# Kernel optimization log

Hardware: AMD Instinct MI355X
Metric: run time of the kernel (lower is better)

The kernel has to match this reference:

```python
import jax, jax.numpy as jnp
import numpy as np

T, H, I, E, K = 2048, 1024, 1024, 16, 4
ALPHA, LIMIT, EPS = 1.702, 7.0, 1e-5


def setup_inputs() -> dict:
    key = jax.random.key(0)
    ks = jax.random.split(key, 8)
    s = 0.02  # init scale for weights
    return {
        "x": jax.random.normal(ks[0], (T, H), jnp.float32),
        "norm_scale": jnp.ones((H,), jnp.float32),
        "gate_w": jax.random.normal(ks[1], (E, H), jnp.float32) * s,
        "gate_b": jax.random.normal(ks[2], (E,), jnp.float32) * s,
        "mlp1_w": jax.random.normal(ks[3], (E, 2 * I, H), jnp.float32) * s,
        "mlp1_b": jax.random.normal(ks[4], (E, 2 * I), jnp.float32) * s,
        "mlp2_w": jax.random.normal(ks[5], (E, H, I), jnp.float32) * s,
        "mlp2_b": jax.random.normal(ks[6], (E, H), jnp.float32) * s,
    }


def rmsnorm(x, scale):
    t = x * jax.lax.rsqrt(jnp.mean(x * x, axis=-1, keepdims=True) + EPS)
    return t * scale


def swiglu(h):
    # interleaved gating: even channels -> glu, odd channels -> linear
    glu = jnp.minimum(h[..., ::2], LIMIT)
    lin = jnp.clip(h[..., 1::2], -LIMIT, LIMIT)
    return glu * jax.nn.sigmoid(ALPHA * glu) * (lin + 1.0)


def reference(x, norm_scale, gate_w, gate_b, mlp1_w, mlp1_b, mlp2_w, mlp2_b):
    t = rmsnorm(x, norm_scale)                                   # [T,H]
    g = t @ gate_w.T + gate_b                                    # [T,E]
    vals, idx = jax.lax.top_k(g, K)                              # [T,K]
    w = jax.nn.softmax(vals, axis=-1)                            # [T,K]
    # Dense per-expert FFN (same math as per-token weight gather, computed
    # once per expert then selected -- avoids materializing [T,K,2I,H]).
    h = jnp.einsum('th,ech->tec', t, mlp1_w) + mlp1_b            # [T,E,2I]
    act = swiglu(h)                                              # [T,E,I]
    y = jnp.einsum('tei,ehi->teh', act, mlp2_w) + mlp2_b         # [T,E,H]
    y_sel = jnp.take_along_axis(y, idx[:, :, None], axis=1)      # [T,K,H]
    return x + jnp.einsum('tkh,tk->th', y_sel, w)
```

## Files before the change

### kernel.cpp

```cpp
#include <hip/hip_runtime.h>
#include <hip/hip_bf16.h>
#include <stdint.h>

typedef unsigned short u16;
typedef __attribute__((ext_vector_type(8))) short short8;
typedef __attribute__((ext_vector_type(4))) float f32x4;

#define T_TOK 2048
#define H_DIM 1024
#define E_NUM 16
#define TWO_I 2048
#define I_DIM 1024
#define ALPHA 1.702f
#define LIMIT 7.0f
#define CNT_STRIDE 64

__device__ __forceinline__ u16 f2b(float f) {
    uint32_t x = __builtin_bit_cast(uint32_t, f);
    uint32_t r = x + 0x7fffu + ((x >> 16) & 1u);
    return (u16)(r >> 16);
}
__device__ __forceinline__ short8 pack8(float4 a, float4 b) {
    short8 r;
    r[0] = (short)f2b(a.x); r[1] = (short)f2b(a.y);
    r[2] = (short)f2b(a.z); r[3] = (short)f2b(a.w);
    r[4] = (short)f2b(b.x); r[5] = (short)f2b(b.y);
    r[6] = (short)f2b(b.z); r[7] = (short)f2b(b.w);
    return r;
}

typedef __attribute__((address_space(1))) void gas_void;
typedef __attribute__((address_space(3))) void las_void;
__device__ __forceinline__ void gl_lds16(const void* g, void* l) {
    __builtin_amdgcn_global_load_lds((gas_void*)g, (las_void*)l, 16, 0, 0);
}

template<typename BT> struct BFrag;
template<> struct BFrag<u16> {
    short8 v;
    __device__ __forceinline__ void load(const u16* p) { v = *(const short8*)p; }
    __device__ __forceinline__ short8 get() const { return v; }
};
template<> struct BFrag<float> {
    float4 a, b;
    __device__ __forceinline__ void load(const float* p) {
        const float4* q = (const float4*)p; a = q[0]; b = q[1];
    }
    __device__ __forceinline__ short8 get() const { return pack8(a, b); }
};

__global__ __launch_bounds__(256) void cvt_kernel(
    const float* __restrict__ in1, u16* __restrict__ out1, int n1,
    const float* __restrict__ in2, u16* __restrict__ out2, int n2)
{
    int i = blockIdx.x * 256 + threadIdx.x;
    int stride = gridDim.x * 256;
    int ntot = n1 + n2;
    for (; i < ntot; i += stride) {
        const float* in; u16* out; int j;
        if (i < n1) { in = in1; out = out1; j = i; }
        else        { in = in2; out = out2; j = i - n1; }
        float4 v = ((const float4*)in)[j];
        uint32_t lo = (uint32_t)f2b(v.x) | ((uint32_t)f2b(v.y) << 16);
        uint32_t hi = (uint32_t)f2b(v.z) | ((uint32_t)f2b(v.w) << 16);
        uint2 p; p.x = lo; p.y = hi;
        ((uint2*)out)[j] = p;
    }
}

__global__ __launch_bounds__(256) void prep_kernel(
    const float* __restrict__ x, const float* __restrict__ scale,
    const float* __restrict__ gw, const float* __restrict__ gb,
    u16* __restrict__ t_out, int* __restrict__ cnt,
    int* __restrict__ pairs, float* __restrict__ pweight,
    float* __restrict__ out)
{
    const int t = blockIdx.x, tid = threadIdx.x;
    const int lane = tid & 63, wid = tid >> 6;
    __shared__ float red[4];
    __shared__ float g4[4][16];
    __shared__ float gsh[16];
    __shared__ float rstd_sh;

    const float4 xv = ((const float4*)(x + (size_t)t * H_DIM))[tid];
    ((float4*)(out + (size_t)t * H_DIM))[tid] = xv;
    float ss = xv.x*xv.x + xv.y*xv.y + xv.z*xv.z + xv.w*xv.w;
#pragma unroll
    for (int off = 32; off > 0; off >>= 1) ss += __shfl_down(ss, off);
    if (lane == 0) red[wid] = ss;
    __syncthreads();
    if (tid == 0) rstd_sh = rsqrtf((red[0]+red[1]+red[2]+red[3]) * (1.f/1024.f) + 1e-5f);
    __syncthreads();
    const float rstd = rstd_sh;
    const float4 sc = ((const float4*)scale)[tid];
    float4 tv;
    tv.x = xv.x * rstd * sc.x; tv.y = xv.y * rstd * sc.y;
    tv.z = xv.z * rstd * sc.z; tv.w = xv.w * rstd * sc.w;
    {
        uint32_t lo = (uint32_t)f2b(tv.x) | ((uint32_t)f2b(tv.y) << 16);
        uint32_t hi = (uint32_t)f2b(tv.z) | ((uint32_t)f2b(tv.w) << 16);
        uint2 p; p.x = lo; p.y = hi;
        *(uint2*)(t_out + (size_t)t * H_DIM + tid * 4) = p;
    }
    float part[16];
#pragma unroll
    for (int e = 0; e < 16; e++) {
        const float4 w4 = ((const float4*)(gw + (size_t)e * H_DIM))[tid];
        part[e] = tv.x*w4.x + tv.y*w4.y + tv.z*w4.z + tv.w*w4.w;
    }
#pragma unroll
    for (int e = 0; e < 16; e++) {
        float v = part[e];
#pragma unroll
        for (int off = 32; off > 0; off >>= 1) v += __shfl_down(v, off);
        if (lane == 0) g4[wid][e] = v;
    }
    __syncthreads();
    if (tid < 16) gsh[tid] = g4[0][tid] + g4[1][tid] + g4[2][tid] + g4[3][tid] + gb[tid];
    __syncthreads();
    if (tid == 0) {
        unsigned mask = 0;
        float vals[4]; int idxs[4];
#pragma unroll
        for (int k = 0; k < 4; k++) {
            float best = -1e30f; int bi = 0;
            for (int e = 0; e < 16; e++)
                if (!((mask >> e) & 1u) && gsh[e] > best) { best = gsh[e]; bi = e; }
            mask |= 1u << bi; vals[k] = best; idxs[k] = bi;
        }
        float m = vals[0], s = 0.f, w[4];
#pragma unroll
        for (int k = 0; k < 4; k++) { w[k] = __expf(vals[k] - m); s += w[k]; }
        float inv = 1.f / s;
#pragma unroll
        for (int k = 0; k < 4; k++) {
            int slot = atomicAdd(&cnt[idxs[k] * CNT_STRIDE], 1);
            pairs[idxs[k] * 2048 + slot] = t * 4 + k;
            pweight[t * 4 + k] = w[k] * inv;
        }
    }
}

template<typename BT>
__global__ __launch_bounds__(256, 1) void ffn1_kernel(
    const u16* __restrict__ t_ws, const BT* __restrict__ w1,
    const float* __restrict__ b1, const int* __restrict__ cnt,
    const int* __restrict__ pairs, u16* __restrict__ act)
{
    const int e = blockIdx.z, nt = blockIdx.x, mt = blockIdx.y;
    const int cnt_e = cnt[e * CNT_STRIDE];
    if (mt * 128 >= cnt_e) return;
    const int tid = threadIdx.x;

    __shared__ u16 As[128 * 64];
    __shared__ u16 Bs[128 * 64];

    const BT* w1e = w1 + (size_t)e * TWO_I * H_DIM;
    const int* plist = pairs + e * 2048;

    const u16* aptr[4]; const BT* bptr[4]; int ldsoff[4];
#pragma unroll
    for (int i = 0; i < 4; i++) {
        int c = tid + i * 256;
        int r = c >> 3, kc = c & 7;
        int kcs = kc ^ (r & 7);
        int gr = mt * 128 + r;
        int info = (gr < cnt_e) ? plist[gr] : plist[0];
        aptr[i] = t_ws + (size_t)(info >> 2) * H_DIM + kcs * 8;
        ldsoff[i] = c * 8;
        int t16 = r >> 4, l16 = r & 15;
        int hcol = nt * 128 + (t16 >> 1) * 32 + l16 * 2 + (t16 & 1);
        bptr[i] = w1e + (size_t)hcol * H_DIM + kcs * 8;
    }

    const int lane = tid & 63, wid = tid >> 6;
    const int wm = wid >> 1, wn = wid & 1;
    const int l15 = lane & 15, quad = lane >> 4;
    const int swz = l15 & 7;

    f32x4 acc[4][4];
#pragma unroll
    for (int mi = 0; mi < 4; mi++)
#pragma unroll
        for (int ni = 0; ni < 4; ni++) acc[mi][ni] = (f32x4){0.f, 0.f, 0.f, 0.f};

    for (int ki = 0; ki < 16; ki++) {
        __syncthreads();
        if constexpr (sizeof(BT) == 2) {
#pragma unroll
            for (int i = 0; i < 4; i++) gl_lds16(aptr[i] + ki * 64, &As[ldsoff[i]]);
#pragma unroll
            for (int i = 0; i < 4; i++) gl_lds16((const BT*)bptr[i] + ki * 64, &Bs[ldsoff[i]]);
        } else {
            short8 ta[4]; BFrag<BT> fb[4];
#pragma unroll
            for (int i = 0; i < 4; i++) ta[i] = *(const short8*)(aptr[i] + ki * 64);
#pragma unroll
            for (int i = 0; i < 4; i++) fb[i].load(bptr[i] + ki * 64);
#pragma unroll
            for (int i = 0; i < 4; i++) *(short8*)(&As[ldsoff[i]]) = ta[i];
#pragma unroll
            for (int i = 0; i < 4; i++) *(short8*)(&Bs[ldsoff[i]]) = fb[i].get();
        }
        __syncthreads();
#pragma unroll
        for (int ks = 0; ks < 2; ks++) {
            short8 af[4], bfr[4];
#pragma unroll
            for (int mi = 0; mi < 4; mi++)
                af[mi] = *(const short8*)(&As[(wm * 64 + mi * 16 + l15) * 64 + (((ks << 2) + quad) ^ swz) * 8]);
#pragma unroll
            for (int ni = 0; ni < 4; ni++)
                bfr[ni] = *(const short8*)(&Bs[(wn * 64 + ni * 16 + l15) * 64 + (((ks << 2) + quad) ^ swz) * 8]);
#pragma unroll
            for (int mi = 0; mi < 4; mi++)
#pragma unroll
                for (int ni = 0; ni < 4; ni++)
                    acc[mi][ni] = __builtin_amdgcn_mfma_f32_16x16x32_bf16(af[mi], bfr[ni], acc[mi][ni], 0, 0, 0);
        }
    }

#pragma unroll
    for (int mi = 0; mi < 4; mi++) {
        int rloc = wm * 64 + mi * 16 + quad * 4;
        int rinfo[4]; bool rval[4];
#pragma unroll
        for (int rg = 0; rg < 4; rg++) {
            int gr = mt * 128 + rloc + rg;
            rval[rg] = gr < cnt_e;
            rinfo[rg] = rval[rg] ? plist[gr] : 0;
        }
#pragma unroll
        for (int qi = 0; qi < 2; qi++) {
            int actcol = nt * 64 + (wn * 2 + qi) * 16 + l15;
            float be = b1[e * TWO_I + 2 * actcol];
            float bo = b1[e * TWO_I + 2 * actcol + 1];
            f32x4 De = acc[mi][qi * 2], Do = acc[mi][qi * 2 + 1];
#pragma unroll
            for (int rg = 0; rg < 4; rg++) {
                if (!rval[rg]) continue;
                float he = De[rg] + be, ho = Do[rg] + bo;
                float glu = fminf(he, LIMIT);
                float lin = fminf(fmaxf(ho, -LIMIT), LIMIT);
                float a = glu * (1.f / (1.f + __expf(-ALPHA * glu))) * (lin + 1.f);
                act[(size_t)rinfo[rg] * I_DIM + actcol] = f2b(a);
            }
        }
    }
}

template<typename BT>
__global__ __launch_bounds__(256, 1) void ffn2_kernel(
    const u16* __restrict__ act, const BT* __restrict__ w2,
    const float* __restrict__ b2, const int* __restrict__ cnt,
    const int* __restrict__ pairs, const float* __restrict__ pweight,
    float* __restrict__ out)
{
    const int e = blockIdx.z, nt = blockIdx.x, mt = blockIdx.y;
    const int cnt_e = cnt[e * CNT_STRIDE];
    if (mt * 128 >= cnt_e) return;
    const int tid = threadIdx.x;

    __shared__ u16 As[128 * 64];
    __shared__ u16 Bs[128 * 64];

    const BT* w2e = w2 + (size_t)e * H_DIM * I_DIM;
    const int* plist = pairs + e * 2048;

    const u16* aptr[4]; const BT* bptr[4]; int ldsoff[4];
#pragma unroll
    for (int i = 0; i < 4; i++) {
        int c = tid + i * 256;
        int r = c >> 3, kc = c & 7;
        int kcs = kc ^ (r & 7);
        int gr = mt * 128 + r;
        int info = (gr < cnt_e) ? plist[gr] : plist[0];
        aptr[i] = act + (size_t)info * I_DIM + kcs * 8;
        ldsoff[i] = c * 8;
        bptr[i] = w2e + (size_t)(nt * 128 + r) * I_DIM + kcs * 8;
    }

    const int lane = tid & 63, wid = tid >> 6;
    const int wm = wid >> 1, wn = wid & 1;
    const int l15 = lane & 15, quad = lane >> 4;
    const int swz = l15 & 7;

    f32x4 acc[4][4];
#pragma unroll
    for (int mi = 0; mi < 4; mi++)
#pragma unroll
        for (int ni = 0; ni < 4; ni++) acc[mi][ni] = (f32x4){0.f, 0.f, 0.f, 0.f};

    for (int ki = 0; ki < 16; ki++) {
        __syncthreads();
        if constexpr (sizeof(BT) == 2) {
#pragma unroll
            for (int i = 0; i < 4; i++) gl_lds16(aptr[i] + ki * 64, &As[ldsoff[i]]);
#pragma unroll
            for (int i = 0; i < 4; i++) gl_lds16((const BT*)bptr[i] + ki * 64, &Bs[ldsoff[i]]);
        } else {
            short8 ta[4]; BFrag<BT> fb[4];
#pragma unroll
            for (int i = 0; i < 4; i++) ta[i] = *(const short8*)(aptr[i] + ki * 64);
#pragma unroll
            for (int i = 0; i < 4; i++) fb[i].load(bptr[i] + ki * 64);
#pragma unroll
            for (int i = 0; i < 4; i++) *(short8*)(&As[ldsoff[i]]) = ta[i];
#pragma unroll
            for (int i = 0; i < 4; i++) *(short8*)(&Bs[ldsoff[i]]) = fb[i].get();
        }
        __syncthreads();
#pragma unroll
        for (int ks = 0; ks < 2; ks++) {
            short8 af[4], bfr[4];
#pragma unroll
            for (int mi = 0; mi < 4; mi++)
                af[mi] = *(const short8*)(&As[(wm * 64 + mi * 16 + l15) * 64 + (((ks << 2) + quad) ^ swz) * 8]);
#pragma unroll
            for (int ni = 0; ni < 4; ni++)
                bfr[ni] = *(const short8*)(&Bs[(wn * 64 + ni * 16 + l15) * 64 + (((ks << 2) + quad) ^ swz) * 8]);
#pragma unroll
            for (int mi = 0; mi < 4; mi++)
#pragma unroll
                for (int ni = 0; ni < 4; ni++)
                    acc[mi][ni] = __builtin_amdgcn_mfma_f32_16x16x32_bf16(af[mi], bfr[ni], acc[mi][ni], 0, 0, 0);
        }
    }

#pragma unroll
    for (int mi = 0; mi < 4; mi++) {
        int rloc = wm * 64 + mi * 16 + quad * 4;
        int rinfo[4]; bool rval[4]; float wp[4];
#pragma unroll
        for (int rg = 0; rg < 4; rg++) {
            int gr = mt * 128 + rloc + rg;
            rval[rg] = gr < cnt_e;
            rinfo[rg] = rval[rg] ? plist[gr] : 0;
            wp[rg] = rval[rg] ? pweight[rinfo[rg]] : 0.f;
        }
#pragma unroll
        for (int ni = 0; ni < 4; ni++) {
            int hc = nt * 128 + wn * 64 + ni * 16 + l15;
            float bv = b2[e * H_DIM + hc];
#pragma unroll
            for (int rg = 0; rg < 4; rg++) {
                if (!rval[rg]) continue;
                float val = (acc[mi][ni][rg] + bv) * wp[rg];
                atomicAdd(&out[(size_t)(rinfo[rg] >> 2) * H_DIM + hc], val);
            }
        }
    }
}

extern "C" void kernel_launch(void* const* d_in, const int* in_sizes, int n_in,
                              void* d_out, int out_size, void* d_ws, size_t ws_size,
                              hipStream_t stream)
{
    const float* x      = (const float*)d_in[0];
    const float* nscale = (const float*)d_in[1];
    const float* gate_w = (const float*)d_in[2];
    const float* gate_b = (const float*)d_in[3];
    const float* mlp1_w = (const float*)d_in[4];
    const float* mlp1_b = (const float*)d_in[5];
    const float* mlp2_w = (const float*)d_in[6];
    const float* mlp2_b = (const float*)d_in[7];
    float* out = (float*)d_out;

    char* ws = (char*)d_ws;
    u16*   t_ws  = (u16*)(ws);
    u16*   act   = (u16*)(ws + (4ull << 20));
    int*   cnt   = (int*)(ws + (28ull << 20));
    int*   pairs = (int*)(ws + (28ull << 20) + 4096);
    float* pw    = (float*)(ws + (28ull << 20) + 4096 + E_NUM * 2048 * 4);
    u16*   w1b   = (u16*)(ws + (32ull << 20));
    u16*   w2b   = (u16*)(ws + (96ull << 20));

    const bool big = ws_size >= (128ull << 20);

    hipMemsetAsync(cnt, 0, E_NUM * CNT_STRIDE * sizeof(int), stream);

    if (big) {
        cvt_kernel<<<2048, 256, 0, stream>>>(mlp1_w, w1b, E_NUM * TWO_I * H_DIM / 4,
                                             mlp2_w, w2b, E_NUM * H_DIM * I_DIM / 4);
    }
    prep_kernel<<<T_TOK, 256, 0, stream>>>(x, nscale, gate_w, gate_b, t_ws, cnt, pairs, pw, out);
    if (big) {
        ffn1_kernel<u16><<<dim3(16, 16, E_NUM), 256, 0, stream>>>(t_ws, w1b, mlp1_b, cnt, pairs, act);
        ffn2_kernel<u16><<<dim3(8, 16, E_NUM), 256, 0, stream>>>(act, w2b, mlp2_b, cnt, pairs, pw, out);
    } else {
        ffn1_kernel<float><<<dim3(16, 16, E_NUM), 256, 0, stream>>>(t_ws, mlp1_w, mlp1_b, cnt, pairs, act);
        ffn2_kernel<float><<<dim3(8, 16, E_NUM), 256, 0, stream>>>(act, mlp2_w, mlp2_b, cnt, pairs, pw, out);
    }
}
```

Baseline: 437.3 us.

## Enlarge FFN GEMM tiles to 256x256 with 512 threads and double-buffered LDS

Both expert GEMM kernels move from 128x128 tiles with 256 threads to 256x256 tiles with 8 waves, each wave holding an 8x4 grid of MFMA accumulators. The global-to-LDS loads are now double-buffered, so the next K slice is prefetched while the current one is computed, and one barrier per iteration is removed. The weight conversion kernel also processes 8 floats per thread with 16-byte stores. The larger tiles improve operand reuse but sharply cut the block count (fewer M tiles per expert, more wasted rows on partial tiles), raise register pressure from 128 accumulator floats, and use 128 KB of LDS.

```diff
diff --git a/kernel.cpp b/kernel.cpp
--- a/kernel.cpp
+++ b/kernel.cpp
@@ -55,16 +55,19 @@
 {
     int i = blockIdx.x * 256 + threadIdx.x;
     int stride = gridDim.x * 256;
-    int ntot = n1 + n2;
-    for (; i < ntot; i += stride) {
+    int p1 = n1 >> 1, ptot = (n1 + n2) >> 1;
+    for (; i < ptot; i += stride) {
         const float* in; u16* out; int j;
-        if (i < n1) { in = in1; out = out1; j = i; }
-        else        { in = in2; out = out2; j = i - n1; }
-        float4 v = ((const float4*)in)[j];
-        uint32_t lo = (uint32_t)f2b(v.x) | ((uint32_t)f2b(v.y) << 16);
-        uint32_t hi = (uint32_t)f2b(v.z) | ((uint32_t)f2b(v.w) << 16);
-        uint2 p; p.x = lo; p.y = hi;
-        ((uint2*)out)[j] = p;
+        if (i < p1) { in = in1; out = out1; j = i; }
+        else        { in = in2; out = out2; j = i - p1; }
+        float4 a = ((const float4*)in)[2 * j];
+        float4 b = ((const float4*)in)[2 * j + 1];
+        uint4 p;
+        p.x = (uint32_t)f2b(a.x) | ((uint32_t)f2b(a.y) << 16);
+        p.y = (uint32_t)f2b(a.z) | ((uint32_t)f2b(a.w) << 16);
+        p.z = (uint32_t)f2b(b.x) | ((uint32_t)f2b(b.y) << 16);
+        p.w = (uint32_t)f2b(b.z) | ((uint32_t)f2b(b.w) << 16);
+        ((uint4*)out)[j] = p;
     }
 }
 
@@ -142,18 +145,18 @@
 }
 
 template<typename BT>
-__global__ __launch_bounds__(256, 1) void ffn1_kernel(
+__global__ __launch_bounds__(512, 1) void ffn1_kernel(
     const u16* __restrict__ t_ws, const BT* __restrict__ w1,
     const float* __restrict__ b1, const int* __restrict__ cnt,
     const int* __restrict__ pairs, u16* __restrict__ act)
 {
     const int e = blockIdx.z, nt = blockIdx.x, mt = blockIdx.y;
     const int cnt_e = cnt[e * CNT_STRIDE];
-    if (mt * 128 >= cnt_e) return;
+    if (mt * 256 >= cnt_e) return;
     const int tid = threadIdx.x;
 
-    __shared__ u16 As[128 * 64];
-    __shared__ u16 Bs[128 * 64];
+    __shared__ u16 As[2][256 * 64];
+    __shared__ u16 Bs[2][256 * 64];
 
     const BT* w1e = w1 + (size_t)e * TWO_I * H_DIM;
     const int* plist = pairs + e * 2048;
@@ -161,78 +164,79 @@
     const u16* aptr[4]; const BT* bptr[4]; int ldsoff[4];
 #pragma unroll
     for (int i = 0; i < 4; i++) {
-        int c = tid + i * 256;
+        int c = tid + i * 512;
         int r = c >> 3, kc = c & 7;
         int kcs = kc ^ (r & 7);
-        int gr = mt * 128 + r;
+        int gr = mt * 256 + r;
         int info = (gr < cnt_e) ? plist[gr] : plist[0];
         aptr[i] = t_ws + (size_t)(info >> 2) * H_DIM + kcs * 8;
         ldsoff[i] = c * 8;
         int t16 = r >> 4, l16 = r & 15;
-        int hcol = nt * 128 + (t16 >> 1) * 32 + l16 * 2 + (t16 & 1);
+        int hcol = nt * 256 + (t16 >> 1) * 32 + l16 * 2 + (t16 & 1);
         bptr[i] = w1e + (size_t)hcol * H_DIM + kcs * 8;
     }
 
     const int lane = tid & 63, wid = tid >> 6;
-    const int wm = wid >> 1, wn = wid & 1;
+    const int wm = wid >> 2, wn = wid & 3;
     const int l15 = lane & 15, quad = lane >> 4;
     const int swz = l15 & 7;
 
-    f32x4 acc[4][4];
-#pragma unroll
-    for (int mi = 0; mi < 4; mi++)
+    f32x4 acc[8][4];
+#pragma unroll
+    for (int mi = 0; mi < 8; mi++)
 #pragma unroll
         for (int ni = 0; ni < 4; ni++) acc[mi][ni] = (f32x4){0.f, 0.f, 0.f, 0.f};
 
+    auto stage = [&](int ki, int buf) {
+#pragma unroll
+        for (int i = 0; i < 4; i++) gl_lds16(aptr[i] + ki * 64, &As[buf][ldsoff[i]]);
+        if constexpr (sizeof(BT) == 2) {
+#pragma unroll
+            for (int i = 0; i < 4; i++) gl_lds16((const u16*)bptr[i] + ki * 64, &Bs[buf][ldsoff[i]]);
+        } else {
+            BFrag<BT> fb[4];
+#pragma unroll
+            for (int i = 0; i < 4; i++) fb[i].load(bptr[i] + ki * 64);
+#pragma unroll
+            for (int i = 0; i < 4; i++) *(short8*)(&Bs[buf][ldsoff[i]]) = fb[i].get();
+        }
+    };
+
+    stage(0, 0);
+    __syncthreads();
     for (int ki = 0; ki < 16; ki++) {
+        const int cur = ki & 1;
+        if (ki < 15) stage(ki + 1, cur ^ 1);
+#pragma unroll
+        for (int ks = 0; ks < 2; ks++) {
+            short8 bfr[4];
+#pragma unroll
+            for (int ni = 0; ni < 4; ni++)
+                bfr[ni] = *(const short8*)(&Bs[cur][(wn * 64 + ni * 16 + l15) * 64 + (((ks << 2) + quad) ^ swz) * 8]);
+#pragma unroll
+            for (int mi = 0; mi < 8; mi++) {
+                short8 af = *(const short8*)(&As[cur][(wm * 128 + mi * 16 + l15) * 64 + (((ks << 2) + quad) ^ swz) * 8]);
+#pragma unroll
+                for (int ni = 0; ni < 4; ni++)
+                    acc[mi][ni] = __builtin_amdgcn_mfma_f32_16x16x32_bf16(af, bfr[ni], acc[mi][ni], 0, 0, 0);
+            }
+        }
         __syncthreads();
-        if constexpr (sizeof(BT) == 2) {
-#pragma unroll
-            for (int i = 0; i < 4; i++) gl_lds16(aptr[i] + ki * 64, &As[ldsoff[i]]);
-#pragma unroll
-            for (int i = 0; i < 4; i++) gl_lds16((const BT*)bptr[i] + ki * 64, &Bs[ldsoff[i]]);
-        } else {
-            short8 ta[4]; BFrag<BT> fb[4];
-#pragma unroll
-            for (int i = 0; i < 4; i++) ta[i] = *(const short8*)(aptr[i] + ki * 64);
-#pragma unroll
-            for (int i = 0; i < 4; i++) fb[i].load(bptr[i] + ki * 64);
-#pragma unroll
-            for (int i = 0; i < 4; i++) *(short8*)(&As[ldsoff[i]]) = ta[i];
-#pragma unroll
-            for (int i = 0; i < 4; i++) *(short8*)(&Bs[ldsoff[i]]) = fb[i].get();
-        }
-        __syncthreads();
-#pragma unroll
-        for (int ks = 0; ks < 2; ks++) {
-            short8 af[4], bfr[4];
-#pragma unroll
-            for (int mi = 0; mi < 4; mi++)
-                af[mi] = *(const short8*)(&As[(wm * 64 + mi * 16 + l15) * 64 + (((ks << 2) + quad) ^ swz) * 8]);
-#pragma unroll
-            for (int ni = 0; ni < 4; ni++)
-                bfr[ni] = *(const short8*)(&Bs[(wn * 64 + ni * 16 + l15) * 64 + (((ks << 2) + quad) ^ swz) * 8]);
-#pragma unroll
-            for (int mi = 0; mi < 4; mi++)
-#pragma unroll
-                for (int ni = 0; ni < 4; ni++)
-                    acc[mi][ni] = __builtin_amdgcn_mfma_f32_16x16x32_bf16(af[mi], bfr[ni], acc[mi][ni], 0, 0, 0);
-        }
-    }
-
-#pragma unroll
-    for (int mi = 0; mi < 4; mi++) {
-        int rloc = wm * 64 + mi * 16 + quad * 4;
+    }
+
+#pragma unroll
+    for (int mi = 0; mi < 8; mi++) {
+        int rloc = wm * 128 + mi * 16 + quad * 4;
         int rinfo[4]; bool rval[4];
 #pragma unroll
         for (int rg = 0; rg < 4; rg++) {
-            int gr = mt * 128 + rloc + rg;
+            int gr = mt * 256 + rloc + rg;
             rval[rg] = gr < cnt_e;
             rinfo[rg] = rval[rg] ? plist[gr] : 0;
         }
 #pragma unroll
         for (int qi = 0; qi < 2; qi++) {
-            int actcol = nt * 64 + (wn * 2 + qi) * 16 + l15;
+            int actcol = nt * 128 + (wn * 2 + qi) * 16 + l15;
             float be = b1[e * TWO_I + 2 * actcol];
             float bo = b1[e * TWO_I + 2 * actcol + 1];
             f32x4 De = acc[mi][qi * 2], Do = acc[mi][qi * 2 + 1];
@@ -250,7 +254,7 @@
 }
 
 template<typename BT>
-__global__ __launch_bounds__(256, 1) void ffn2_kernel(
+__global__ __launch_bounds__(512, 1) void ffn2_kernel(
     const u16* __restrict__ act, const BT* __restrict__ w2,
     const float* __restrict__ b2, const int* __restrict__ cnt,
     const int* __restrict__ pairs, const float* __restrict__ pweight,
@@ -258,11 +262,11 @@
 {
     const int e = blockIdx.z, nt = blockIdx.x, mt = blockIdx.y;
     const int cnt_e = cnt[e * CNT_STRIDE];
-    if (mt * 128 >= cnt_e) return;
+    if (mt * 256 >= cnt_e) return;
     const int tid = threadIdx.x;
 
-    __shared__ u16 As[128 * 64];
-    __shared__ u16 Bs[128 * 64];
+    __shared__ u16 As[2][256 * 64];
+    __shared__ u16 Bs[2][256 * 64];
 
     const BT* w2e = w2 + (size_t)e * H_DIM * I_DIM;
     const int* plist = pairs + e * 2048;
@@ -270,77 +274,78 @@
     const u16* aptr[4]; const BT* bptr[4]; int ldsoff[4];
 #pragma unroll
     for (int i = 0; i < 4; i++) {
-        int c = tid + i * 256;
+        int c = tid + i * 512;
         int r = c >> 3, kc = c & 7;
         int kcs = kc ^ (r & 7);
-        int gr = mt * 128 + r;
+        int gr = mt * 256 + r;
         int info = (gr < cnt_e) ? plist[gr] : plist[0];
         aptr[i] = act + (size_t)info * I_DIM + kcs * 8;
         ldsoff[i] = c * 8;
-        bptr[i] = w2e + (size_t)(nt * 128 + r) * I_DIM + kcs * 8;
+        bptr[i] = w2e + (size_t)(nt * 256 + r) * I_DIM + kcs * 8;
     }
 
     const int lane = tid & 63, wid = tid >> 6;
-    const int wm = wid >> 1, wn = wid & 1;
+    const int wm = wid >> 2, wn = wid & 3;
     const int l15 = lane & 15, quad = lane >> 4;
     const int swz = l15 & 7;
 
-    f32x4 acc[4][4];
-#pragma unroll
-    for (int mi = 0; mi < 4; mi++)
+    f32x4 acc[8][4];
+#pragma unroll
+    for (int mi = 0; mi < 8; mi++)
 #pragma unroll
         for (int ni = 0; ni < 4; ni++) acc[mi][ni] = (f32x4){0.f, 0.f, 0.f, 0.f};
 
+    auto stage = [&](int ki, int buf) {
+#pragma unroll
+        for (int i = 0; i < 4; i++) gl_lds16(aptr[i] + ki * 64, &As[buf][ldsoff[i]]);
+        if constexpr (sizeof(BT) == 2) {
+#pragma unroll
+            for (int i = 0; i < 4; i++) gl_lds16((const u16*)bptr[i] + ki * 64, &Bs[buf][ldsoff[i]]);
+        } else {
+            BFrag<BT> fb[4];
+#pragma unroll
+            for (int i = 0; i < 4; i++) fb[i].load(bptr[i] + ki * 64);
+#pragma unroll
+            for (int i = 0; i < 4; i++) *(short8*)(&Bs[buf][ldsoff[i]]) = fb[i].get();
+        }
+    };
+
+    stage(0, 0);
+    __syncthreads();
     for (int ki = 0; ki < 16; ki++) {
+        const int cur = ki & 1;
+        if (ki < 15) stage(ki + 1, cur ^ 1);
+#pragma unroll
+        for (int ks = 0; ks < 2; ks++) {
+            short8 bfr[4];
+#pragma unroll
+            for (int ni = 0; ni < 4; ni++)
+                bfr[ni] = *(const short8*)(&Bs[cur][(wn * 64 + ni * 16 + l15) * 64 + (((ks << 2) + quad) ^ swz) * 8]);
+#pragma unroll
+            for (int mi = 0; mi < 8; mi++) {
+                short8 af = *(const short8*)(&As[cur][(wm * 128 + mi * 16 + l15) * 64 + (((ks << 2) + quad) ^ swz) * 8]);
+#pragma unroll
+                for (int ni = 0; ni < 4; ni++)
+                    acc[mi][ni] = __builtin_amdgcn_mfma_f32_16x16x32_bf16(af, bfr[ni], acc[mi][ni], 0, 0, 0);
+            }
+        }
         __syncthreads();
-        if constexpr (sizeof(BT) == 2) {
-#pragma unroll
-            for (int i = 0; i < 4; i++) gl_lds16(aptr[i] + ki * 64, &As[ldsoff[i]]);
-#pragma unroll
-            for (int i = 0; i < 4; i++) gl_lds16((const BT*)bptr[i] + ki * 64, &Bs[ldsoff[i]]);
-        } else {
-            short8 ta[4]; BFrag<BT> fb[4];
-#pragma unroll
-            for (int i = 0; i < 4; i++) ta[i] = *(const short8*)(aptr[i] + ki * 64);
-#pragma unroll
-            for (int i = 0; i < 4; i++) fb[i].load(bptr[i] + ki * 64);
-#pragma unroll
-            for (int i = 0; i < 4; i++) *(short8*)(&As[ldsoff[i]]) = ta[i];
-#pragma unroll
-            for (int i = 0; i < 4; i++) *(short8*)(&Bs[ldsoff[i]]) = fb[i].get();
-        }
-        __syncthreads();
-#pragma unroll
-        for (int ks = 0; ks < 2; ks++) {
-            short8 af[4], bfr[4];
-#pragma unroll
-            for (int mi = 0; mi < 4; mi++)
-                af[mi] = *(const short8*)(&As[(wm * 64 + mi * 16 + l15) * 64 + (((ks << 2) + quad) ^ swz) * 8]);
-#pragma unroll
-            for (int ni = 0; ni < 4; ni++)
-                bfr[ni] = *(const short8*)(&Bs[(wn * 64 + ni * 16 + l15) * 64 + (((ks << 2) + quad) ^ swz) * 8]);
-#pragma unroll
-            for (int mi = 0; mi < 4; mi++)
-#pragma unroll
-                for (int ni = 0; ni < 4; ni++)
-                    acc[mi][ni] = __builtin_amdgcn_mfma_f32_16x16x32_bf16(af[mi], bfr[ni], acc[mi][ni], 0, 0, 0);
-        }
-    }
-
-#pragma unroll
-    for (int mi = 0; mi < 4; mi++) {
-        int rloc = wm * 64 + mi * 16 + quad * 4;
+    }
+
+#pragma unroll
+    for (int mi = 0; mi < 8; mi++) {
+        int rloc = wm * 128 + mi * 16 + quad * 4;
         int rinfo[4]; bool rval[4]; float wp[4];
 #pragma unroll
         for (int rg = 0; rg < 4; rg++) {
-            int gr = mt * 128 + rloc + rg;
+            int gr = mt * 256 + rloc + rg;
             rval[rg] = gr < cnt_e;
             rinfo[rg] = rval[rg] ? plist[gr] : 0;
             wp[rg] = rval[rg] ? pweight[rinfo[rg]] : 0.f;
         }
 #pragma unroll
         for (int ni = 0; ni < 4; ni++) {
-            int hc = nt * 128 + wn * 64 + ni * 16 + l15;
+            int hc = nt * 256 + wn * 64 + ni * 16 + l15;
             float bv = b2[e * H_DIM + hc];
 #pragma unroll
             for (int rg = 0; rg < 4; rg++) {
@@ -385,10 +390,10 @@
     }
     prep_kernel<<<T_TOK, 256, 0, stream>>>(x, nscale, gate_w, gate_b, t_ws, cnt, pairs, pw, out);
     if (big) {
-        ffn1_kernel<u16><<<dim3(16, 16, E_NUM), 256, 0, stream>>>(t_ws, w1b, mlp1_b, cnt, pairs, act);
-        ffn2_kernel<u16><<<dim3(8, 16, E_NUM), 256, 0, stream>>>(act, w2b, mlp2_b, cnt, pairs, pw, out);
+        ffn1_kernel<u16><<<dim3(8, 8, E_NUM), 512, 0, stream>>>(t_ws, w1b, mlp1_b, cnt, pairs, act);
+        ffn2_kernel<u16><<<dim3(4, 8, E_NUM), 512, 0, stream>>>(act, w2b, mlp2_b, cnt, pairs, pw, out);
     } else {
-        ffn1_kernel<float><<<dim3(16, 16, E_NUM), 256, 0, stream>>>(t_ws, mlp1_w, mlp1_b, cnt, pairs, act);
-        ffn2_kernel<float><<<dim3(8, 16, E_NUM), 256, 0, stream>>>(act, mlp2_w, mlp2_b, cnt, pairs, pw, out);
-    }
-}
+        ffn1_kernel<float><<<dim3(8, 8, E_NUM), 512, 0, stream>>>(t_ws, mlp1_w, mlp1_b, cnt, pairs, act);
+        ffn2_kernel<float><<<dim3(4, 8, E_NUM), 512, 0, stream>>>(act, mlp2_w, mlp2_b, cnt, pairs, pw, out);
+    }
+}
```

Measured after the change: 542.6 us. +24.1%, slower.

## Drop fp32-to-bf16 weight pre-conversion pass and prefetch fp32 weights in registers

Applied to the files above, without the earlier changes.

Removes the separate conversion kernel that rewrote all expert weights to bf16 in workspace every call. The FFN kernels now read fp32 weights directly, converting in registers. They prefetch the next K-slice of weights into registers while the MFMAs for the current slice run, and tokens are loaded asynchronously into LDS. This avoids reading the full weight set an extra time and writing a bf16 copy, at the cost of doubled weight bytes inside the GEMMs, more register pressure, and ALU conversion work in the inner loop.

```diff
diff --git a/kernel.cpp b/kernel.cpp
--- a/kernel.cpp
+++ b/kernel.cpp
@@ -35,38 +35,13 @@
     __builtin_amdgcn_global_load_lds((gas_void*)g, (las_void*)l, 16, 0, 0);
 }
 
-template<typename BT> struct BFrag;
-template<> struct BFrag<u16> {
-    short8 v;
-    __device__ __forceinline__ void load(const u16* p) { v = *(const short8*)p; }
-    __device__ __forceinline__ short8 get() const { return v; }
-};
-template<> struct BFrag<float> {
+struct BFragF {
     float4 a, b;
     __device__ __forceinline__ void load(const float* p) {
         const float4* q = (const float4*)p; a = q[0]; b = q[1];
     }
     __device__ __forceinline__ short8 get() const { return pack8(a, b); }
 };
-
-__global__ __launch_bounds__(256) void cvt_kernel(
-    const float* __restrict__ in1, u16* __restrict__ out1, int n1,
-    const float* __restrict__ in2, u16* __restrict__ out2, int n2)
-{
-    int i = blockIdx.x * 256 + threadIdx.x;
-    int stride = gridDim.x * 256;
-    int ntot = n1 + n2;
-    for (; i < ntot; i += stride) {
-        const float* in; u16* out; int j;
-        if (i < n1) { in = in1; out = out1; j = i; }
-        else        { in = in2; out = out2; j = i - n1; }
-        float4 v = ((const float4*)in)[j];
-        uint32_t lo = (uint32_t)f2b(v.x) | ((uint32_t)f2b(v.y) << 16);
-        uint32_t hi = (uint32_t)f2b(v.z) | ((uint32_t)f2b(v.w) << 16);
-        uint2 p; p.x = lo; p.y = hi;
-        ((uint2*)out)[j] = p;
-    }
-}
 
 __global__ __launch_bounds__(256) void prep_kernel(
     const float* __restrict__ x, const float* __restrict__ scale,
@@ -141,9 +116,8 @@
     }
 }
 
-template<typename BT>
 __global__ __launch_bounds__(256, 1) void ffn1_kernel(
-    const u16* __restrict__ t_ws, const BT* __restrict__ w1,
+    const u16* __restrict__ t_ws, const float* __restrict__ w1,
     const float* __restrict__ b1, const int* __restrict__ cnt,
     const int* __restrict__ pairs, u16* __restrict__ act)
 {
@@ -155,10 +129,10 @@
     __shared__ u16 As[128 * 64];
     __shared__ u16 Bs[128 * 64];
 
-    const BT* w1e = w1 + (size_t)e * TWO_I * H_DIM;
+    const float* w1e = w1 + (size_t)e * TWO_I * H_DIM;
     const int* plist = pairs + e * 2048;
 
-    const u16* aptr[4]; const BT* bptr[4]; int ldsoff[4];
+    const u16* aptr[4]; const float* bptr[4]; int ldsA[4], ldsB[4];
 #pragma unroll
     for (int i = 0; i < 4; i++) {
         int c = tid + i * 256;
@@ -167,10 +141,11 @@
         int gr = mt * 128 + r;
         int info = (gr < cnt_e) ? plist[gr] : plist[0];
         aptr[i] = t_ws + (size_t)(info >> 2) * H_DIM + kcs * 8;
-        ldsoff[i] = c * 8;
+        ldsA[i] = c * 8;
         int t16 = r >> 4, l16 = r & 15;
         int hcol = nt * 128 + (t16 >> 1) * 32 + l16 * 2 + (t16 & 1);
-        bptr[i] = w1e + (size_t)hcol * H_DIM + kcs * 8;
+        bptr[i] = w1e + (size_t)hcol * H_DIM + kc * 8;
+        ldsB[i] = r * 64 + kcs * 8;
     }
 
     const int lane = tid & 63, wid = tid >> 6;
@@ -184,25 +159,21 @@
 #pragma unroll
         for (int ni = 0; ni < 4; ni++) acc[mi][ni] = (f32x4){0.f, 0.f, 0.f, 0.f};
 
+    BFragF fb[4];
+#pragma unroll
+    for (int i = 0; i < 4; i++) fb[i].load(bptr[i]);
+
     for (int ki = 0; ki < 16; ki++) {
         __syncthreads();
-        if constexpr (sizeof(BT) == 2) {
-#pragma unroll
-            for (int i = 0; i < 4; i++) gl_lds16(aptr[i] + ki * 64, &As[ldsoff[i]]);
-#pragma unroll
-            for (int i = 0; i < 4; i++) gl_lds16((const BT*)bptr[i] + ki * 64, &Bs[ldsoff[i]]);
-        } else {
-            short8 ta[4]; BFrag<BT> fb[4];
-#pragma unroll
-            for (int i = 0; i < 4; i++) ta[i] = *(const short8*)(aptr[i] + ki * 64);
-#pragma unroll
-            for (int i = 0; i < 4; i++) fb[i].load(bptr[i] + ki * 64);
-#pragma unroll
-            for (int i = 0; i < 4; i++) *(short8*)(&As[ldsoff[i]]) = ta[i];
-#pragma unroll
-            for (int i = 0; i < 4; i++) *(short8*)(&Bs[ldsoff[i]]) = fb[i].get();
-        }
+#pragma unroll
+        for (int i = 0; i < 4; i++) gl_lds16(aptr[i] + ki * 64, &As[ldsA[i]]);
+#pragma unroll
+        for (int i = 0; i < 4; i++) *(short8*)(&Bs[ldsB[i]]) = fb[i].get();
         __syncthreads();
+        if (ki < 15) {
+#pragma unroll
+            for (int i = 0; i < 4; i++) fb[i].load(bptr[i] + (ki + 1) * 64);
+        }
 #pragma unroll
         for (int ks = 0; ks < 2; ks++) {
             short8 af[4], bfr[4];
@@ -249,9 +220,8 @@
     }
 }
 
-template<typename BT>
 __global__ __launch_bounds__(256, 1) void ffn2_kernel(
-    const u16* __restrict__ act, const BT* __restrict__ w2,
+    const u16* __restrict__ act, const float* __restrict__ w2,
     const float* __restrict__ b2, const int* __restrict__ cnt,
     const int* __restrict__ pairs, const float* __restrict__ pweight,
     float* __restrict__ out)
@@ -264,10 +234,10 @@
     __shared__ u16 As[128 * 64];
     __shared__ u16 Bs[128 * 64];
 
-    const BT* w2e = w2 + (size_t)e * H_DIM * I_DIM;
+    const float* w2e = w2 + (size_t)e * H_DIM * I_DIM;
     const int* plist = pairs + e * 2048;
 
-    const u16* aptr[4]; const BT* bptr[4]; int ldsoff[4];
+    const u16* aptr[4]; const float* bptr[4]; int ldsA[4], ldsB[4];
 #pragma unroll
     for (int i = 0; i < 4; i++) {
         int c = tid + i * 256;
@@ -276,8 +246,9 @@
         int gr = mt * 128 + r;
         int info = (gr < cnt_e) ? plist[gr] : plist[0];
         aptr[i] = act + (size_t)info * I_DIM + kcs * 8;
-        ldsoff[i] = c * 8;
-        bptr[i] = w2e + (size_t)(nt * 128 + r) * I_DIM + kcs * 8;
+        ldsA[i] = c * 8;
+        bptr[i] = w2e + (size_t)(nt * 128 + r) * I_DIM + kc * 8;
+        ldsB[i] = r * 64 + kcs * 8;
     }
 
     const int lane = tid & 63, wid = tid >> 6;
@@ -291,25 +262,21 @@
 #pragma unroll
         for (int ni = 0; ni < 4; ni++) acc[mi][ni] = (f32x4){0.f, 0.f, 0.f, 0.f};
 
+    BFragF fb[4];
+#pragma unroll
+    for (int i = 0; i < 4; i++) fb[i].load(bptr[i]);
+
     for (int ki = 0; ki < 16; ki++) {
         __syncthreads();
-        if constexpr (sizeof(BT) == 2) {
-#pragma unroll
-            for (int i = 0; i < 4; i++) gl_lds16(aptr[i] + ki * 64, &As[ldsoff[i]]);
-#pragma unroll
-            for (int i = 0; i < 4; i++) gl_lds16((const BT*)bptr[i] + ki * 64, &Bs[ldsoff[i]]);
-        } else {
-            short8 ta[4]; BFrag<BT> fb[4];
-#pragma unroll
-            for (int i = 0; i < 4; i++) ta[i] = *(const short8*)(aptr[i] + ki * 64);
-#pragma unroll
-            for (int i = 0; i < 4; i++) fb[i].load(bptr[i] + ki * 64);
-#pragma unroll
-            for (int i = 0; i < 4; i++) *(short8*)(&As[ldsoff[i]]) = ta[i];
-#pragma unroll
-            for (int i = 0; i < 4; i++) *(short8*)(&Bs[ldsoff[i]]) = fb[i].get();
-        }
+#pragma unroll
+        for (int i = 0; i < 4; i++) gl_lds16(aptr[i] + ki * 64, &As[ldsA[i]]);
+#pragma unroll
+        for (int i = 0; i < 4; i++) *(short8*)(&Bs[ldsB[i]]) = fb[i].get();
         __syncthreads();
+        if (ki < 15) {
+#pragma unroll
+            for (int i = 0; i < 4; i++) fb[i].load(bptr[i] + (ki + 1) * 64);
+        }
 #pragma unroll
         for (int ks = 0; ks < 2; ks++) {
             short8 af[4], bfr[4];
@@ -369,26 +336,13 @@
     char* ws = (char*)d_ws;
     u16*   t_ws  = (u16*)(ws);
     u16*   act   = (u16*)(ws + (4ull << 20));
-    int*   cnt   = (int*)(ws + (28ull << 20));
-    int*   pairs = (int*)(ws + (28ull << 20) + 4096);
-    float* pw    = (float*)(ws + (28ull << 20) + 4096 + E_NUM * 2048 * 4);
-    u16*   w1b   = (u16*)(ws + (32ull << 20));
-    u16*   w2b   = (u16*)(ws + (96ull << 20));
-
-    const bool big = ws_size >= (128ull << 20);
+    int*   cnt   = (int*)(ws + (20ull << 20));
+    int*   pairs = (int*)(ws + (20ull << 20) + 4096);
+    float* pw    = (float*)(ws + (20ull << 20) + 4096 + E_NUM * 2048 * 4);
 
     hipMemsetAsync(cnt, 0, E_NUM * CNT_STRIDE * sizeof(int), stream);
 
-    if (big) {
-        cvt_kernel<<<2048, 256, 0, stream>>>(mlp1_w, w1b, E_NUM * TWO_I * H_DIM / 4,
-                                             mlp2_w, w2b, E_NUM * H_DIM * I_DIM / 4);
-    }
     prep_kernel<<<T_TOK, 256, 0, stream>>>(x, nscale, gate_w, gate_b, t_ws, cnt, pairs, pw, out);
-    if (big) {
-        ffn1_kernel<u16><<<dim3(16, 16, E_NUM), 256, 0, stream>>>(t_ws, w1b, mlp1_b, cnt, pairs, act);
-        ffn2_kernel<u16><<<dim3(8, 16, E_NUM), 256, 0, stream>>>(act, w2b, mlp2_b, cnt, pairs, pw, out);
-    } else {
-        ffn1_kernel<float><<<dim3(16, 16, E_NUM), 256, 0, stream>>>(t_ws, mlp1_w, mlp1_b, cnt, pairs, act);
-        ffn2_kernel<float><<<dim3(8, 16, E_NUM), 256, 0, stream>>>(act, mlp2_w, mlp2_b, cnt, pairs, pw, out);
-    }
-}
+    ffn1_kernel<<<dim3(16, 16, E_NUM), 256, 0, stream>>>(t_ws, mlp1_w, mlp1_b, cnt, pairs, act);
+    ffn2_kernel<<<dim3(8, 16, E_NUM), 256, 0, stream>>>(act, mlp2_w, mlp2_b, cnt, pairs, pw, out);
+}
```

After: 429.8 us. About the same (-1.7%).
